# Kernel optimization log

Hardware: AMD Instinct MI355X
Metric: run time of the kernel (lower is better)

The kernel has to match this reference:

```python
import jax, jax.numpy as jnp
import numpy as np
import math

NUM_HEADS = 32
KV_CHANNELS = 128
LAYER_NUMBER = 4
# apply_query_key_layer_scaling=True: norm_factor = sqrt(head_dim) * layer_number,
# then scores are re-multiplied by layer_number in fp32 (numerics trick).
NORM_FACTOR = math.sqrt(KV_CHANNELS) * LAYER_NUMBER
COEFF = float(LAYER_NUMBER)
NEG = -1e9


def setup_inputs() -> dict:
    key = jax.random.key(0)
    k1, k2, k3 = jax.random.split(key, 3)
    b, h, s, d = 2, NUM_HEADS, 2048, KV_CHANNELS
    q = jax.random.normal(k1, (b, h, s, d), dtype=jnp.float32)
    k = jax.random.normal(k2, (b, h, s, d), dtype=jnp.float32)
    v = jax.random.normal(k3, (b, h, s, d), dtype=jnp.float32)
    # additive causal mask: 0 where allowed (j <= i), large negative where masked
    causal = jnp.tril(jnp.ones((s, s), dtype=bool))
    mask = jnp.where(causal, 0.0, NEG).astype(jnp.float32)[None, None, :, :]
    mask = jnp.broadcast_to(mask, (b, 1, s, s))
    return {"query_layer": q, "key_layer": k, "value_layer": v, "attention_mask": mask}


def reference(query_layer, key_layer, value_layer, attention_mask):
    b, h, sq, d = query_layer.shape
    skv = key_layer.shape[2]
    # baddbmm with beta=0, alpha=1/norm_factor  ==  (Q K^T) / norm_factor
    scores = jnp.einsum('bhqd,bhkd->bhqk', query_layer, key_layer) / NORM_FACTOR
    # attention_softmax_in_fp32 + layer scaling coefficient
    scores = scores.astype(jnp.float32) * COEFF
    scores = scores + attention_mask[:, :, :, :skv]
    probs = jax.nn.softmax(scores, axis=-1).astype(value_layer.dtype)
    # dropout p=0.0 -> identity
    context = jnp.einsum('bhqk,bhkd->bhqd', probs, value_layer)
    # transpose to [b, sq, h, d] then merge heads -> [b, sq, h*d]
    context = context.transpose(0, 2, 1, 3).reshape(b, sq, h * d)
    return context
```

## Files before the change

### kernel.cpp

```cpp
#include <hip/hip_runtime.h>
#include <cstdint>
#include <cstddef>

typedef __attribute__((ext_vector_type(8))) __bf16 bf16x8;
typedef __attribute__((ext_vector_type(4))) __bf16 bf16x4;
typedef __attribute__((ext_vector_type(4))) float f32x4;

#define SEQ 2048
#define DIM 128
#define NHEAD 32
#define NBATCH 2
#define NHEADS_TOTAL (NHEAD * NBATCH)
#define SCALE 0.08838834764831845f
#define QSC (0.08838834764831845f * 1.4426950408889634f)

#define KV_TILE 32
#define TILES_PER_HEAD (SEQ / KV_TILE)
#define TILE_ELEMS (KV_TILE * DIM)
#define K_WS_BYTES ((size_t)NHEADS_TOTAL * TILES_PER_HEAD * TILE_ELEMS * 2)
#define WS_NEEDED (2 * K_WS_BYTES)

#define PS 40

__device__ __forceinline__ float fexp2(float x) {
#if __has_builtin(__builtin_amdgcn_exp2f)
  return __builtin_amdgcn_exp2f(x);
#else
  return __expf(x * 0.69314718055994531f);
#endif
}

__global__ __launch_bounds__(256) void glm_prepass(const float* __restrict__ Kg,
                                                   const float* __restrict__ Vg,
                                                   __bf16* __restrict__ Kws,
                                                   __bf16* __restrict__ Vws) {
  __shared__ float Vl[32 * 132];
  const int hd = blockIdx.x >> 6;
  const int t  = blockIdx.x & 63;
  const int i  = threadIdx.x;
  const int kv = i >> 3, seg = i & 7;
  const size_t src   = ((size_t)hd * SEQ + (size_t)t * 32 + kv) * DIM + seg * 16;
  const size_t tbase = (size_t)(hd * TILES_PER_HEAD + t) * TILE_ELEMS;

  {
    f32x4 a = *(const f32x4*)(Kg + src);
    f32x4 b = *(const f32x4*)(Kg + src + 4);
    f32x4 c4 = *(const f32x4*)(Kg + src + 8);
    f32x4 d4 = *(const f32x4*)(Kg + src + 12);
    bf16x8 A, B;
#pragma unroll
    for (int j = 0; j < 4; ++j) {
      A[j] = (__bf16)a[j]; A[4 + j] = (__bf16)b[j];
      B[j] = (__bf16)c4[j]; B[4 + j] = (__bf16)d4[j];
    }
    const int cf = kv >> 4, lc = kv & 15, cc = seg >> 1, q0 = (seg & 1) * 2;
    const int chunkA = (cf * 4 + cc) * 64 + q0 * 16 + lc;
    *(bf16x8*)&Kws[tbase + (size_t)chunkA * 8] = A;
    *(bf16x8*)&Kws[tbase + (size_t)(chunkA + 16) * 8] = B;
  }

  {
    f32x4 a = *(const f32x4*)(Vg + src);
    f32x4 b = *(const f32x4*)(Vg + src + 4);
    f32x4 c4 = *(const f32x4*)(Vg + src + 8);
    f32x4 d4 = *(const f32x4*)(Vg + src + 12);
    float* vl = &Vl[kv * 132 + seg * 16];
    *(f32x4*)(vl + 0) = a; *(f32x4*)(vl + 4) = b;
    *(f32x4*)(vl + 8) = c4; *(f32x4*)(vl + 12) = d4;
  }
  __syncthreads();
#pragma unroll
  for (int u = 0; u < 2; ++u) {
    const int ch = i * 2 + u;
    const int nt = ch >> 6, kvg = (ch >> 4) & 3, dd = ch & 15;
    bf16x8 wv;
#pragma unroll
    for (int e = 0; e < 8; ++e) wv[e] = (__bf16)Vl[(kvg * 8 + e) * 132 + nt * 16 + dd];
    *(bf16x8*)&Vws[tbase + (size_t)ch * 8] = wv;
  }
}

__global__ __launch_bounds__(256, 2) void glm_attn_main(const float* __restrict__ Qg,
                                                        const __bf16* __restrict__ Kws,
                                                        const __bf16* __restrict__ Vws,
                                                        float* __restrict__ Out) {
  __shared__ __align__(16) __bf16 Kb[TILE_ELEMS];
  __shared__ __align__(16) __bf16 Vb[TILE_ELEMS];
  __shared__ __align__(16) __bf16 Pt[4][32 * PS];

  const int tid  = threadIdx.x;
  const int w    = tid >> 6;
  const int lane = tid & 63;
  const int quad = lane >> 4;
  const int lcol = lane & 15;

  const int qx = (int)gridDim.x - 1 - (int)blockIdx.x;
  const int qb = qx * 128;
  const int hi = blockIdx.y, bi = blockIdx.z;
  const int hd = bi * NHEAD + hi;

  const float*  Qh   = Qg + (size_t)hd * SEQ * DIM;
  const __bf16* Ksrc = Kws + (size_t)hd * TILES_PER_HEAD * TILE_ELEMS;
  const __bf16* Vsrc = Vws + (size_t)hd * TILES_PER_HEAD * TILE_ELEMS;

  bf16x8 qf[2][4];
#pragma unroll
  for (int m = 0; m < 2; ++m) {
    const float* qp = Qh + (size_t)(qb + w * 32 + m * 16 + lcol) * DIM + quad * 8;
#pragma unroll
    for (int c = 0; c < 4; ++c) {
      f32x4 a = *(const f32x4*)(qp + c * 32);
      f32x4 b = *(const f32x4*)(qp + c * 32 + 4);
      bf16x8 t;
#pragma unroll
      for (int j = 0; j < 4; ++j) {
        t[j] = (__bf16)(a[j] * QSC);
        t[4 + j] = (__bf16)(b[j] * QSC);
      }
      qf[m][c] = t;
    }
  }

  f32x4 o[2][8];
#pragma unroll
  for (int m = 0; m < 2; ++m)
#pragma unroll
    for (int n = 0; n < 8; ++n) o[m][n] = f32x4{0.f, 0.f, 0.f, 0.f};
  float lsum[2][4];
#pragma unroll
  for (int m = 0; m < 2; ++m)
#pragma unroll
    for (int r = 0; r < 4; ++r) lsum[m][r] = 0.0f;

  const int T = qx * 4 + 4;
  const int Tfull = qx * 4;

  bf16x8 kst0, kst1, vst0, vst1;
  {
    const __bf16* ks = Ksrc + (size_t)tid * 8;
    const __bf16* vs = Vsrc + (size_t)tid * 8;
    kst0 = *(const bf16x8*)ks;        kst1 = *(const bf16x8*)(ks + 2048);
    vst0 = *(const bf16x8*)vs;        vst1 = *(const bf16x8*)(vs + 2048);
  }

  for (int t = 0; t < T; ++t) {
    __syncthreads();
    *(bf16x8*)&Kb[tid * 8]        = kst0;
    *(bf16x8*)&Kb[tid * 8 + 2048] = kst1;
    *(bf16x8*)&Vb[tid * 8]        = vst0;
    *(bf16x8*)&Vb[tid * 8 + 2048] = vst1;
    __syncthreads();
    if (t + 1 < T) {
      const __bf16* ks = Ksrc + (size_t)(t + 1) * TILE_ELEMS + (size_t)tid * 8;
      const __bf16* vs = Vsrc + (size_t)(t + 1) * TILE_ELEMS + (size_t)tid * 8;
      kst0 = *(const bf16x8*)ks;      kst1 = *(const bf16x8*)(ks + 2048);
      vst0 = *(const bf16x8*)vs;      vst1 = *(const bf16x8*)(vs + 2048);
    }

    f32x4 s[2][2];
    s[0][0] = s[0][1] = s[1][0] = s[1][1] = f32x4{0.f, 0.f, 0.f, 0.f};
#pragma unroll
    for (int c = 0; c < 4; ++c) {
      bf16x8 k0 = *(const bf16x8*)&Kb[c * 512 + lane * 8];
      bf16x8 k1 = *(const bf16x8*)&Kb[(4 + c) * 512 + lane * 8];
      s[0][0] = __builtin_amdgcn_mfma_f32_16x16x32_bf16(qf[0][c], k0, s[0][0], 0, 0, 0);
      s[1][0] = __builtin_amdgcn_mfma_f32_16x16x32_bf16(qf[1][c], k0, s[1][0], 0, 0, 0);
      s[0][1] = __builtin_amdgcn_mfma_f32_16x16x32_bf16(qf[0][c], k1, s[0][1], 0, 0, 0);
      s[1][1] = __builtin_amdgcn_mfma_f32_16x16x32_bf16(qf[1][c], k1, s[1][1], 0, 0, 0);
    }

    __bf16* pw = Pt[w];
    if (t < Tfull) {
#pragma unroll
      for (int m = 0; m < 2; ++m)
#pragma unroll
        for (int cf = 0; cf < 2; ++cf)
#pragma unroll
          for (int r = 0; r < 4; ++r) {
            const float p = fexp2(fminf(s[m][cf][r], 30.0f));
            lsum[m][r] += p;
            pw[(m * 16 + quad * 4 + r) * PS + cf * 16 + lcol] = (__bf16)p;
          }
    } else {
      const int kvb = t * 32;
#pragma unroll
      for (int m = 0; m < 2; ++m) {
        const int rowb = qb + w * 32 + m * 16 + quad * 4;
#pragma unroll
        for (int cf = 0; cf < 2; ++cf) {
          const int col = kvb + cf * 16 + lcol;
#pragma unroll
          for (int r = 0; r < 4; ++r) {
            const float p = (col <= rowb + r) ? fexp2(fminf(s[m][cf][r], 30.0f)) : 0.0f;
            lsum[m][r] += p;
            pw[(m * 16 + quad * 4 + r) * PS + cf * 16 + lcol] = (__bf16)p;
          }
        }
      }
    }

    bf16x8 pf0 = *(const bf16x8*)&pw[lcol * PS + quad * 8];
    bf16x8 pf1 = *(const bf16x8*)&pw[(16 + lcol) * PS + quad * 8];
#pragma unroll
    for (int nt = 0; nt < 8; ++nt) {
      bf16x8 vf = *(const bf16x8*)&Vb[nt * 512 + lane * 8];
      o[0][nt] = __builtin_amdgcn_mfma_f32_16x16x32_bf16(pf0, vf, o[0][nt], 0, 0, 0);
      o[1][nt] = __builtin_amdgcn_mfma_f32_16x16x32_bf16(pf1, vf, o[1][nt], 0, 0, 0);
    }
  }

#pragma unroll
  for (int m = 0; m < 2; ++m)
#pragma unroll
    for (int r = 0; r < 4; ++r) {
      float v = lsum[m][r];
      v += __shfl_xor(v, 1); v += __shfl_xor(v, 2);
      v += __shfl_xor(v, 4); v += __shfl_xor(v, 8);
      lsum[m][r] = 1.0f / v;
    }
#pragma unroll
  for (int m = 0; m < 2; ++m) {
    const int row0 = qb + w * 32 + m * 16 + quad * 4;
#pragma unroll
    for (int r = 0; r < 4; ++r) {
      const float inv = lsum[m][r];
      float* op = Out + ((size_t)bi * SEQ + row0 + r) * (NHEAD * DIM) + hi * DIM + lcol;
#pragma unroll
      for (int nt = 0; nt < 8; ++nt) op[nt * 16] = o[m][nt][r] * inv;
    }
  }
}

#define KT_S 136
#define VT_S 40
#define PT_S 40

__global__ __launch_bounds__(256, 1) void glm_attn(const float* __restrict__ Qg,
                                                   const float* __restrict__ Kg,
                                                   const float* __restrict__ Vg,
                                                   float* __restrict__ Out) {
  __shared__ __align__(16) __bf16 Kt[32 * KT_S];
  __shared__ __align__(16) __bf16 Vt[128 * VT_S];
  __shared__ __align__(16) __bf16 Pa[4][16 * PT_S];

  const int tid  = threadIdx.x;
  const int wave = tid >> 6;
  const int lane = tid & 63;
  const int quad = lane >> 4;
  const int lcol = lane & 15;

  const int qbb = blockIdx.x * 64;
  const int hi = blockIdx.y;
  const int bi = blockIdx.z;

  const size_t head = ((size_t)(bi * NHEAD + hi)) * SEQ * DIM;
  const float* Qh = Qg + head;
  const float* Kh = Kg + head;
  const float* Vh = Vg + head;

  bf16x8 qf[4];
  {
    const int qrow = qbb + wave * 16 + lcol;
    const float* qp = Qh + (size_t)qrow * DIM + quad * 8;
    for (int c = 0; c < 4; ++c) {
      bf16x8 t;
      for (int j = 0; j < 8; ++j) t[j] = (__bf16)qp[c * 32 + j];
      qf[c] = t;
    }
  }

  f32x4 o[8];
  for (int n = 0; n < 8; ++n) o[n] = f32x4{0.f, 0.f, 0.f, 0.f};
  float m_r[4], l_r[4];
  for (int r = 0; r < 4; ++r) { m_r[r] = -3.0e38f; l_r[r] = 0.0f; }

  const int row0 = qbb + wave * 16 + quad * 4;
  const int ntiles = (int)blockIdx.x * 2 + 2;
  for (int t = 0; t < ntiles; ++t) {
    const int kvb = t * 32;
    __syncthreads();
    {
      const int r  = tid >> 3;
      const int c0 = (tid & 7) * 16;
      const f32x4* kp4 = (const f32x4*)(Kh + (size_t)(kvb + r) * DIM + c0);
      f32x4 ka = kp4[0], kb = kp4[1], kc = kp4[2], kd = kp4[3];
      bf16x8 lo, hi8;
      for (int j = 0; j < 4; ++j) {
        lo[j] = (__bf16)ka[j]; lo[4 + j] = (__bf16)kb[j];
        hi8[j] = (__bf16)kc[j]; hi8[4 + j] = (__bf16)kd[j];
      }
      *(bf16x8*)&Kt[r * KT_S + c0]     = lo;
      *(bf16x8*)&Kt[r * KT_S + c0 + 8] = hi8;
    }
    {
      const int kvg = (tid >> 5) * 4;
      const int dg  = (tid & 31) * 4;
      f32x4 rowv[4];
      for (int i = 0; i < 4; ++i)
        rowv[i] = *(const f32x4*)(Vh + (size_t)(kvb + kvg + i) * DIM + dg);
      for (int j = 0; j < 4; ++j) {
        bf16x4 wv;
        for (int i = 0; i < 4; ++i) wv[i] = (__bf16)rowv[i][j];
        *(bf16x4*)&Vt[(dg + j) * VT_S + kvg] = wv;
      }
    }
    __syncthreads();

    f32x4 s0 = f32x4{0.f, 0.f, 0.f, 0.f};
    f32x4 s1 = f32x4{0.f, 0.f, 0.f, 0.f};
    for (int c = 0; c < 4; ++c) {
      bf16x8 k0 = *(const bf16x8*)&Kt[lcol * KT_S + c * 32 + quad * 8];
      s0 = __builtin_amdgcn_mfma_f32_16x16x32_bf16(qf[c], k0, s0, 0, 0, 0);
      bf16x8 k1 = *(const bf16x8*)&Kt[(16 + lcol) * KT_S + c * 32 + quad * 8];
      s1 = __builtin_amdgcn_mfma_f32_16x16x32_bf16(qf[c], k1, s1, 0, 0, 0);
    }

    const int c0g = kvb + lcol;
    const int c1g = kvb + 16 + lcol;
    float p0[4], p1[4];
    for (int r = 0; r < 4; ++r) {
      const int rg = row0 + r;
      float v0 = s0[r] * SCALE;
      float v1 = s1[r] * SCALE;
      if (c0g > rg) v0 = -3.0e38f;
      if (c1g > rg) v1 = -3.0e38f;
      float tm = fmaxf(v0, v1);
      tm = fmaxf(tm, __shfl_xor(tm, 1));
      tm = fmaxf(tm, __shfl_xor(tm, 2));
      tm = fmaxf(tm, __shfl_xor(tm, 4));
      tm = fmaxf(tm, __shfl_xor(tm, 8));
      const float mn = fmaxf(m_r[r], tm);
      const float alpha = __expf(m_r[r] - mn);
      m_r[r] = mn;
      const float e0 = __expf(v0 - mn);
      const float e1 = __expf(v1 - mn);
      p0[r] = e0; p1[r] = e1;
      float rs = e0 + e1;
      rs += __shfl_xor(rs, 1);
      rs += __shfl_xor(rs, 2);
      rs += __shfl_xor(rs, 4);
      rs += __shfl_xor(rs, 8);
      l_r[r] = l_r[r] * alpha + rs;
      for (int n = 0; n < 8; ++n) o[n][r] *= alpha;
    }

    __bf16* pw = Pa[wave];
    for (int r = 0; r < 4; ++r) {
      pw[(quad * 4 + r) * PT_S + lcol]      = (__bf16)p0[r];
      pw[(quad * 4 + r) * PT_S + 16 + lcol] = (__bf16)p1[r];
    }
    bf16x8 pf = *(const bf16x8*)&pw[lcol * PT_S + quad * 8];

    for (int n = 0; n < 8; ++n) {
      bf16x8 vf = *(const bf16x8*)&Vt[(n * 16 + lcol) * VT_S + quad * 8];
      o[n] = __builtin_amdgcn_mfma_f32_16x16x32_bf16(pf, vf, o[n], 0, 0, 0);
    }
  }

  float inv_l[4];
  for (int r = 0; r < 4; ++r) inv_l[r] = 1.0f / l_r[r];
  for (int n = 0; n < 8; ++n) {
    const int col = n * 16 + lcol;
    for (int r = 0; r < 4; ++r) {
      const int row = row0 + r;
      Out[(((size_t)bi * SEQ + row) * NHEAD + hi) * DIM + col] = o[n][r] * inv_l[r];
    }
  }
}

extern "C" void kernel_launch(void* const* d_in, const int* in_sizes, int n_in,
                              void* d_out, int out_size, void* d_ws, size_t ws_size,
                              hipStream_t stream) {
  const float* Q = (const float*)d_in[0];
  const float* K = (const float*)d_in[1];
  const float* V = (const float*)d_in[2];
  float* Out = (float*)d_out;

  if (ws_size >= WS_NEEDED) {
    __bf16* Kws = (__bf16*)d_ws;
    __bf16* Vws = (__bf16*)((char*)d_ws + K_WS_BYTES);
    glm_prepass<<<dim3(NHEADS_TOTAL * TILES_PER_HEAD), 256, 0, stream>>>(K, V, Kws, Vws);
    glm_attn_main<<<dim3(SEQ / 128, NHEAD, NBATCH), 256, 0, stream>>>(Q, Kws, Vws, Out);
  } else {
    glm_attn<<<dim3(SEQ / 64, NHEAD, NBATCH), 256, 0, stream>>>(Q, K, V, Out);
  }
}
```

Measured before the change: 378.7 us.

## Remap attention blocks to balance causal work, raise occupancy, streamline V transpose

The main attention kernel now launches on a flat 1D grid and decodes each block id into batch, head and query tile. Four groups of 256 blocks each use a different query-tile ordering, so long causal tiles and short ones are interleaved across the CUs. Launch bounds move from 2 to 4 blocks per CU to allow more resident waves, at the cost of tighter register limits and possible spills. The prepass transposes V into a bf16 LDS tile with padded stride, so the workspace write becomes one vector LDS read per chunk instead of eight scalar reads and converts.

Measured after the change: 458.3 us. 21.0% more time.

```diff
diff --git a/kernel.cpp b/kernel.cpp
--- a/kernel.cpp
+++ b/kernel.cpp
@@ -34,15 +34,16 @@
                                                    const float* __restrict__ Vg,
                                                    __bf16* __restrict__ Kws,
                                                    __bf16* __restrict__ Vws) {
-  __shared__ float Vl[32 * 132];
+  __shared__ __align__(16) __bf16 Vt[128 * 40];
   const int hd = blockIdx.x >> 6;
   const int t  = blockIdx.x & 63;
   const int i  = threadIdx.x;
-  const int kv = i >> 3, seg = i & 7;
-  const size_t src   = ((size_t)hd * SEQ + (size_t)t * 32 + kv) * DIM + seg * 16;
-  const size_t tbase = (size_t)(hd * TILES_PER_HEAD + t) * TILE_ELEMS;
+  const size_t rowbase = (size_t)hd * SEQ + (size_t)t * 32;
+  const size_t tbase   = (size_t)(hd * TILES_PER_HEAD + t) * TILE_ELEMS;
 
   {
+    const int kv = i >> 3, seg = i & 7;
+    const size_t src = (rowbase + kv) * DIM + seg * 16;
     f32x4 a = *(const f32x4*)(Kg + src);
     f32x4 b = *(const f32x4*)(Kg + src + 4);
     f32x4 c4 = *(const f32x4*)(Kg + src + 8);
@@ -60,27 +61,31 @@
   }
 
   {
-    f32x4 a = *(const f32x4*)(Vg + src);
-    f32x4 b = *(const f32x4*)(Vg + src + 4);
-    f32x4 c4 = *(const f32x4*)(Vg + src + 8);
-    f32x4 d4 = *(const f32x4*)(Vg + src + 12);
-    float* vl = &Vl[kv * 132 + seg * 16];
-    *(f32x4*)(vl + 0) = a; *(f32x4*)(vl + 4) = b;
-    *(f32x4*)(vl + 8) = c4; *(f32x4*)(vl + 12) = d4;
+    const int kvg4 = (i >> 5) * 4;
+    const int dg   = (i & 31) * 4;
+    f32x4 rowv[4];
+#pragma unroll
+    for (int j = 0; j < 4; ++j)
+      rowv[j] = *(const f32x4*)(Vg + (rowbase + kvg4 + j) * DIM + dg);
+#pragma unroll
+    for (int j = 0; j < 4; ++j) {
+      bf16x4 w;
+#pragma unroll
+      for (int e = 0; e < 4; ++e) w[e] = (__bf16)rowv[e][j];
+      *(bf16x4*)&Vt[(dg + j) * 40 + kvg4] = w;
+    }
   }
   __syncthreads();
 #pragma unroll
   for (int u = 0; u < 2; ++u) {
-    const int ch = i * 2 + u;
+    const int ch = i + u * 256;
     const int nt = ch >> 6, kvg = (ch >> 4) & 3, dd = ch & 15;
-    bf16x8 wv;
-#pragma unroll
-    for (int e = 0; e < 8; ++e) wv[e] = (__bf16)Vl[(kvg * 8 + e) * 132 + nt * 16 + dd];
-    *(bf16x8*)&Vws[tbase + (size_t)ch * 8] = wv;
+    bf16x8 w = *(const bf16x8*)&Vt[(nt * 16 + dd) * 40 + kvg * 8];
+    *(bf16x8*)&Vws[tbase + (size_t)ch * 8] = w;
   }
 }
 
-__global__ __launch_bounds__(256, 2) void glm_attn_main(const float* __restrict__ Qg,
+__global__ __launch_bounds__(256, 4) void glm_attn_main(const float* __restrict__ Qg,
                                                         const __bf16* __restrict__ Kws,
                                                         const __bf16* __restrict__ Vws,
                                                         float* __restrict__ Out) {
@@ -94,9 +99,20 @@
   const int quad = lane >> 4;
   const int lcol = lane & 15;
 
-  const int qx = (int)gridDim.x - 1 - (int)blockIdx.x;
+  const int id = (int)blockIdx.x;
+  const int g  = id >> 8;
+  const int a  = id & 15;
+  const int cy = (id >> 4) & 15;
+  const int bi = g >> 1;
+  const int hi = cy | ((g & 1) << 4);
+  int qx;
+  switch (g) {
+    case 0:  qx = a; break;
+    case 1:  qx = 15 - a; break;
+    case 2:  qx = (a + 4) & 15; break;
+    default: qx = (11 - a) & 15; break;
+  }
   const int qb = qx * 128;
-  const int hi = blockIdx.y, bi = blockIdx.z;
   const int hd = bi * NHEAD + hi;
 
   const float*  Qh   = Qg + (size_t)hd * SEQ * DIM;
@@ -109,13 +125,13 @@
     const float* qp = Qh + (size_t)(qb + w * 32 + m * 16 + lcol) * DIM + quad * 8;
 #pragma unroll
     for (int c = 0; c < 4; ++c) {
-      f32x4 a = *(const f32x4*)(qp + c * 32);
-      f32x4 b = *(const f32x4*)(qp + c * 32 + 4);
+      f32x4 aa = *(const f32x4*)(qp + c * 32);
+      f32x4 bb = *(const f32x4*)(qp + c * 32 + 4);
       bf16x8 t;
 #pragma unroll
       for (int j = 0; j < 4; ++j) {
-        t[j] = (__bf16)(a[j] * QSC);
-        t[4 + j] = (__bf16)(b[j] * QSC);
+        t[j] = (__bf16)(aa[j] * QSC);
+        t[4 + j] = (__bf16)(bb[j] * QSC);
       }
       qf[m][c] = t;
     }
@@ -380,7 +396,7 @@
     __bf16* Kws = (__bf16*)d_ws;
     __bf16* Vws = (__bf16*)((char*)d_ws + K_WS_BYTES);
     glm_prepass<<<dim3(NHEADS_TOTAL * TILES_PER_HEAD), 256, 0, stream>>>(K, V, Kws, Vws);
-    glm_attn_main<<<dim3(SEQ / 128, NHEAD, NBATCH), 256, 0, stream>>>(Q, Kws, Vws, Out);
+    glm_attn_main<<<dim3(SEQ / 128 * NHEAD * NBATCH), 256, 0, stream>>>(Q, Kws, Vws, Out);
   } else {
     glm_attn<<<dim3(SEQ / 64, NHEAD, NBATCH), 256, 0, stream>>>(Q, K, V, Out);
   }
```
